# Kernel tuning notes

Hardware: AMD Instinct MI355X
Metric: run time of the kernel (lower is better)

The kernel has to match this reference:

```python
import jax, jax.numpy as jnp
import numpy as np

N_NEAR = 16
BN_EPS = 1e-5


def fps(xyz, n_center):
    # farthest point sampling, deterministic start at index 0. xyz: [B,N,C]
    B, N, _ = xyz.shape
    dist0 = jnp.full((B, N), jnp.inf, dtype=xyz.dtype)
    far0 = jnp.zeros((B,), dtype=jnp.int32)

    def step(carry, _):
        dist, far = carry
        centroid = jnp.take_along_axis(xyz, far[:, None, None], axis=1)  # [B,1,C]
        d = jnp.sum((xyz - centroid) ** 2, axis=-1)                       # [B,N]
        dist = jnp.minimum(dist, d)
        nxt = jnp.argmax(dist, axis=-1).astype(jnp.int32)
        return (dist, nxt), far

    _, idxs = jax.lax.scan(step, (dist0, far0), None, length=n_center)
    return jnp.transpose(idxs)  # [B, n_center]


def knn(xyz, k):
    # k nearest neighbors (self included), xyz: [B,N,C] -> idx [B,N,k]
    sq = jnp.sum(xyz * xyz, axis=-1)
    d = sq[:, :, None] - 2.0 * jnp.einsum('bnc,bmc->bnm', xyz, xyz) + sq[:, None, :]
    _, idx = jax.lax.top_k(-d, k)
    return idx


def gather_points(x, idx):
    # x: [B,N,...], idx: [B,*dims] int -> [B,*dims,...]
    return jax.vmap(lambda xb, ib: xb[ib])(x, idx)


def conv_bn_relu(x, W, b, g, be):
    # x: [B,C,K,S]; 1x1 Conv2d + BatchNorm2d (training/batch stats) + ReLU
    y = jnp.einsum('oc,bcks->boks', W, x) + b[None, :, None, None]
    mean = jnp.mean(y, axis=(0, 2, 3), keepdims=True)
    var = jnp.mean((y - mean) ** 2, axis=(0, 2, 3), keepdims=True)  # biased var, as torch BN
    y = (y - mean) * jax.lax.rsqrt(var + BN_EPS)
    y = y * g[None, :, None, None] + be[None, :, None, None]
    return jax.nn.relu(y)


def setup_inputs() -> dict:
    key = jax.random.key(0)
    ks = jax.random.split(key, 8)
    B, N, EMB = 16, 2048, 64
    mlp = [64, 128, 256]
    in_ch = 2 + EMB
    inp = {
        'xy': jax.random.normal(ks[0], (B, 2, N), dtype=jnp.float32),
        'fea': jax.random.normal(ks[1], (B, EMB, N), dtype=jnp.float32),
    }
    last = in_ch
    for i, out in enumerate(mlp):
        inp[f'W{i+1}'] = 0.1 * jax.random.normal(ks[2 + i], (out, last), dtype=jnp.float32)
        inp[f'b{i+1}'] = jnp.zeros((out,), dtype=jnp.float32)
        inp[f'g{i+1}'] = jnp.ones((out,), dtype=jnp.float32)
        inp[f'be{i+1}'] = jnp.zeros((out,), dtype=jnp.float32)
        last = out
    return inp


def reference(xy, fea, W1, b1, g1, be1, W2, b2, g2, be2, W3, b3, g3, be3):
    B, _, N = xy.shape
    n_center = N // 2 + 1
    xyz = jnp.transpose(xy, (0, 2, 1))   # [B,N,2]
    f = jnp.transpose(fea, (0, 2, 1))    # [B,N,emb]

    fps_idx = fps(xyz, n_center)                      # [B,S]
    new_xyz = gather_points(xyz, fps_idx)             # [B,S,2]
    knn_idx = knn(xyz, N_NEAR)                        # [B,N,k]
    knn_of_fps = gather_points(knn_idx, fps_idx)      # [B,S,k]
    grouped_xyz = gather_points(xyz, knn_of_fps)      # [B,S,k,2]
    grouped_norm = grouped_xyz - new_xyz[:, :, None, :]
    grouped_f = gather_points(f, knn_of_fps)          # [B,S,k,emb]
    new_fea = jnp.concatenate([grouped_norm, grouped_f], axis=-1)  # [B,S,k,C]

    x = jnp.transpose(new_fea, (0, 3, 2, 1))          # [B,C,k,S]
    for (W, b, g, be) in ((W1, b1, g1, be1), (W2, b2, g2, be2), (W3, b3, g3, be3)):
        x = conv_bn_relu(x, W, b, g, be)
    out = jnp.max(x, axis=2)                          # [B,C_out,S]
    return jnp.transpose(new_xyz, (0, 2, 1)), out
```

## Files before the change

### kernel.cpp

```cpp
#include <hip/hip_runtime.h>
#include <math.h>

#define B_   16
#define N_   2048
#define S_   1025
#define K_   16
#define EMB_ 64
#define NF_  (B_ * S_ * K_)
#define NCH_ (NF_ / 64)

typedef float v2f __attribute__((ext_vector_type(2)));
typedef short bf16x8 __attribute__((ext_vector_type(8)));
typedef float f32x4 __attribute__((ext_vector_type(4)));

__device__ __forceinline__ unsigned short f2bf(float f) {
  unsigned u = __float_as_uint(f);
  u += 0x7fffu + ((u >> 16) & 1u);
  return (unsigned short)(u >> 16);
}

__global__ __launch_bounds__(256) __attribute__((amdgpu_waves_per_eu(1, 1)))
void fps_pk_kernel(const float* __restrict__ xy, const float* __restrict__ fea,
                   const float* __restrict__ W1,
                   const float* __restrict__ W2, const float* __restrict__ W3,
                   int* __restrict__ fps_idx, float* __restrict__ new_xyz,
                   float* __restrict__ out0, float* __restrict__ P,
                   unsigned short* __restrict__ W2b, unsigned short* __restrict__ W3b) {
  __shared__ float smem[8192];
  if (blockIdx.x < 16) {
    const int b = blockIdx.x;
    float2* lxy = reinterpret_cast<float2*>(smem);
    const int lane = threadIdx.x;
    const float* xb = xy + (size_t)b * 2 * N_;
    v2f pxp[16], pyp[16];
    float dist[32];
    if (lane < 64) {
      const float2* xb2 = (const float2*)xb;
      const float2* yb2 = (const float2*)(xb + N_);
#pragma unroll
      for (int q = 0; q < 16; ++q) {
        float2 x01 = xb2[lane * 16 + q];
        float2 y01 = yb2[lane * 16 + q];
        int p = lane * 32 + 2 * q;
        lxy[p] = make_float2(x01.x, y01.x);
        lxy[p + 1] = make_float2(x01.y, y01.y);
        pxp[q][0] = x01.x; pxp[q][1] = x01.y;
        pyp[q][0] = y01.x; pyp[q][1] = y01.y;
        dist[2 * q] = __builtin_inff();
        dist[2 * q + 1] = __builtin_inff();
      }
#pragma unroll
      for (int q = 0; q < 16; ++q) {
        asm volatile("" : "+v"(pxp[q]), "+v"(pyp[q]));
      }
    }
    __syncthreads();
    if (lane < 64) {
      int cur = 0;
      for (int t = 0; t < S_; ++t) {
        float2 c = lxy[cur];
        if (lane == 0) {
          fps_idx[b * S_ + t] = cur;
          new_xyz[(b * S_ + t) * 2 + 0] = c.x;
          new_xyz[(b * S_ + t) * 2 + 1] = c.y;
          out0[b * 2 * S_ + t] = c.x;
          out0[b * 2 * S_ + S_ + t] = c.y;
        }
        const float ncx = -c.x, ncy = -c.y;
        v2f ncx2; ncx2[0] = ncx; ncx2[1] = ncx;
        v2f ncy2; ncy2[0] = ncy; ncy2[1] = ncy;
#pragma unroll
        for (int q = 0; q < 16; ++q) {
          v2f dx, dy, sx, sy, dd;
          asm("v_pk_add_f32 %0, %1, %2" : "=v"(dx) : "v"(pxp[q]), "v"(ncx2));
          asm("v_pk_add_f32 %0, %1, %2" : "=v"(dy) : "v"(pyp[q]), "v"(ncy2));
          asm("v_pk_mul_f32 %0, %1, %1" : "=v"(sx) : "v"(dx));
          asm("v_pk_mul_f32 %0, %1, %1" : "=v"(sy) : "v"(dy));
          asm("v_pk_add_f32 %0, %1, %2" : "=v"(dd) : "v"(sx), "v"(sy));
          dist[2 * q] = fminf(dist[2 * q], dd[0]);
          dist[2 * q + 1] = fminf(dist[2 * q + 1], dd[1]);
        }
        float m1[16], m2[8], m3[4], m4[2];
#pragma unroll
        for (int j = 0; j < 16; ++j) m1[j] = fmaxf(dist[2 * j], dist[2 * j + 1]);
#pragma unroll
        for (int j = 0; j < 8; ++j) m2[j] = fmaxf(m1[2 * j], m1[2 * j + 1]);
#pragma unroll
        for (int j = 0; j < 4; ++j) m3[j] = fmaxf(m2[2 * j], m2[2 * j + 1]);
        m4[0] = fmaxf(m3[0], m3[1]);
        m4[1] = fmaxf(m3[2], m3[3]);
        const float lmax = fmaxf(m4[0], m4[1]);
        int xr = __float_as_int(lmax);
#define DPP_MAX_STEP(CTRL)                                                        \
        {                                                                         \
          int tmp_ = __builtin_amdgcn_update_dpp(xr, xr, (CTRL), 0xF, 0xF, false);\
          xr = __float_as_int(fmaxf(__int_as_float(xr), __int_as_float(tmp_)));   \
        }
        DPP_MAX_STEP(0x111)
        DPP_MAX_STEP(0x112)
        DPP_MAX_STEP(0x114)
        DPP_MAX_STEP(0x118)
        DPP_MAX_STEP(0x142)
        DPP_MAX_STEP(0x143)
#undef DPP_MAX_STEP
        const float g = __int_as_float(__builtin_amdgcn_readlane(xr, 63));
        int n = (m4[0] == g) ? 0 : 1;
        float c3 = (n & 1) ? m3[2] : m3[0];
        n = 2 * n + ((c3 == g) ? 0 : 1);
        float lo2 = (n & 1) ? m2[2] : m2[0];
        float hi2 = (n & 1) ? m2[6] : m2[4];
        float c2 = (n & 2) ? hi2 : lo2;
        n = 2 * n + ((c2 == g) ? 0 : 1);
        float a0 = (n & 1) ? m1[2] : m1[0];
        float a1 = (n & 1) ? m1[6] : m1[4];
        float a2 = (n & 1) ? m1[10] : m1[8];
        float a3 = (n & 1) ? m1[14] : m1[12];
        float b0 = (n & 2) ? a1 : a0;
        float b1 = (n & 2) ? a3 : a2;
        float c1 = (n & 4) ? b1 : b0;
        n = 2 * n + ((c1 == g) ? 0 : 1);
        float e0 = (n & 1) ? dist[2] : dist[0];
        float e1 = (n & 1) ? dist[6] : dist[4];
        float e2 = (n & 1) ? dist[10] : dist[8];
        float e3 = (n & 1) ? dist[14] : dist[12];
        float e4 = (n & 1) ? dist[18] : dist[16];
        float e5 = (n & 1) ? dist[22] : dist[20];
        float e6 = (n & 1) ? dist[26] : dist[24];
        float e7 = (n & 1) ? dist[30] : dist[28];
        float f0 = (n & 2) ? e1 : e0;
        float f1 = (n & 2) ? e3 : e2;
        float f2 = (n & 2) ? e5 : e4;
        float f3 = (n & 2) ? e7 : e6;
        float g0 = (n & 4) ? f1 : f0;
        float g1 = (n & 4) ? f3 : f2;
        float c0 = (n & 8) ? g1 : g0;
        const int lf = 2 * n + ((c0 == g) ? 0 : 1);
        unsigned long long mask = __ballot(lmax == g);
        int first = __ffsll(mask) - 1;
        cur = __builtin_amdgcn_readlane(lane * 32 + lf, first);
      }
    }
  } else if (blockIdx.x < 528) {
    const int bid = blockIdx.x - 16;
    const int t = threadIdx.x;
    const int b = bid >> 5;
    const int pt0 = (bid & 31) << 6;
    float* W1L = smem;
    float* feaL = smem + 4096;
#pragma unroll
    for (int p = 0; p < 16; ++p) {
      int idx = t + 256 * p;
      int c = idx >> 6, e = idx & 63;
      W1L[e * 64 + c] = W1[c * 66 + 2 + e];
      int r = (t >> 6) + 4 * p, cc = t & 63;
      feaL[r * 64 + cc] = fea[((size_t)b * 64 + r) * N_ + pt0 + cc];
    }
    __syncthreads();
    const int tpt = t & 15, tcq = t >> 4;
    float acc[4][4];
#pragma unroll
    for (int i = 0; i < 4; ++i)
#pragma unroll
      for (int j = 0; j < 4; ++j) acc[i][j] = 0.f;
    for (int e = 0; e < 64; ++e) {
      float4 a4 = *reinterpret_cast<const float4*>(&W1L[e * 64 + tcq * 4]);
      float4 b4 = *reinterpret_cast<const float4*>(&feaL[e * 64 + tpt * 4]);
      const float av[4] = {a4.x, a4.y, a4.z, a4.w};
      const float bvv[4] = {b4.x, b4.y, b4.z, b4.w};
#pragma unroll
      for (int i = 0; i < 4; ++i)
#pragma unroll
        for (int j = 0; j < 4; ++j) acc[i][j] = fmaf(av[i], bvv[j], acc[i][j]);
    }
#pragma unroll
    for (int j = 0; j < 4; ++j) {
      int pt = tpt * 4 + j;
      float4 v = {acc[0][j], acc[1][j], acc[2][j], acc[3][j]};
      *reinterpret_cast<float4*>(&P[((size_t)(b * N_ + pt0 + pt)) * 64 + tcq * 4]) = v;
    }
  } else {
    const int t = threadIdx.x;
    for (int i = t; i < 128 * 64; i += 256) W2b[i] = f2bf(W2[i]);
    for (int i = t; i < 256 * 128; i += 256) W3b[i] = f2bf(W3[i]);
  }
}

__global__ __launch_bounds__(256) void knn_kernel(const float* __restrict__ xy,
                                                  const int* __restrict__ fps_idx,
                                                  int* __restrict__ knn_sel) {
  const int b = blockIdx.y;
  __shared__ float2 lxy[N_];
  __shared__ double lsq[N_];
  const float* xb = xy + (size_t)b * 2 * N_;
  for (int p = threadIdx.x; p < N_; p += 256) {
    float x = xb[p], y = xb[N_ + p];
    lxy[p] = make_float2(x, y);
    lsq[p] = (double)x * (double)x + (double)y * (double)y;
  }
  __syncthreads();
  const int t = threadIdx.x;
  const int s = blockIdx.x * 8 + (t >> 5);
  if (s >= S_) return;
  const int oct = t & 31;
  const int p0 = fps_idx[b * S_ + s];
  float2 q = lxy[p0];
  const double xn = (double)q.x, yn = (double)q.y;
  const double sqn = lsq[p0];
  double d16[16];
  int i16[16];
#pragma unroll
  for (int j = 0; j < 16; ++j) { d16[j] = __builtin_inf(); i16[j] = 0x7fffffff; }
  const int mlo = oct * 64;
  for (int m0 = mlo; m0 < mlo + 64; m0 += 4) {
    double dd[4];
#pragma unroll
    for (int u = 0; u < 4; ++u) {
      float2 p = lxy[m0 + u];
      double dot = (double)p.x * xn + (double)p.y * yn;
      dd[u] = (sqn - 2.0 * dot) + lsq[m0 + u];
    }
#pragma unroll
    for (int u = 0; u < 4; ++u) {
      if (dd[u] < d16[15]) {
        double d = dd[u];
        int mi = m0 + u;
#pragma unroll
        for (int j = 15; j >= 1; --j) {
          bool shift = d < d16[j - 1];
          bool ins = d < d16[j];
          d16[j] = shift ? d16[j - 1] : (ins ? d : d16[j]);
          i16[j] = shift ? i16[j - 1] : (ins ? mi : i16[j]);
        }
        if (d < d16[0]) { d16[0] = d; i16[0] = mi; }
      }
    }
  }
#pragma unroll
  for (int w = 1; w <= 16; w <<= 1) {
    double nd[16]; int ni[16];
#pragma unroll
    for (int i = 0; i < 16; ++i) {
      double rd = __shfl_xor(d16[15 - i], w, 64);
      int ri = __shfl_xor(i16[15 - i], w, 64);
      bool takeR = (rd < d16[i]) || (rd == d16[i] && ri < i16[i]);
      nd[i] = takeR ? rd : d16[i];
      ni[i] = takeR ? ri : i16[i];
    }
#pragma unroll
    for (int i = 0; i < 16; ++i) { d16[i] = nd[i]; i16[i] = ni[i]; }
    if (w < 16) {
#pragma unroll
      for (int dstg = 8; dstg >= 1; dstg >>= 1) {
#pragma unroll
        for (int i = 0; i < 16; ++i) {
          if ((i & dstg) == 0) {
            int a = i, c = i + dstg;
            bool sw = (d16[a] > d16[c]) || (d16[a] == d16[c] && i16[a] > i16[c]);
            double tlo = sw ? d16[c] : d16[a];
            double thi = sw ? d16[a] : d16[c];
            int ulo = sw ? i16[c] : i16[a];
            int uhi = sw ? i16[a] : i16[c];
            d16[a] = tlo; d16[c] = thi; i16[a] = ulo; i16[c] = uhi;
          }
        }
      }
    }
  }
  if (oct == 0) {
    int* dst = knn_sel + ((size_t)b * S_ + s) * K_;
#pragma unroll
    for (int j = 0; j < 16; ++j) dst[j] = i16[j];
  }
}

__global__ __launch_bounds__(256) void yk1_kernel(const float* __restrict__ xy,
                                                  const int* __restrict__ knn_sel,
                                                  const float* __restrict__ new_xyz,
                                                  const float* __restrict__ P,
                                                  const float* __restrict__ W1,
                                                  const float* __restrict__ b1,
                                                  float* __restrict__ Y1) {
  __shared__ float w0s[64], w1s[64], bbs[64];
  const int t = threadIdx.x;
  if (t < 64) { w0s[t] = W1[t * 66 + 0]; w1s[t] = W1[t * 66 + 1]; bbs[t] = b1[t]; }
  __syncthreads();
  const int n = blockIdx.x * 256 + t;
  const int bs = n >> 4;
  const int b = bs / S_;
  const int nbr = knn_sel[n];
  const float dx = xy[(size_t)b * 2 * N_ + nbr] - new_xyz[bs * 2 + 0];
  const float dy = xy[(size_t)b * 2 * N_ + N_ + nbr] - new_xyz[bs * 2 + 1];
  const float* prow = &P[((size_t)(b * N_ + nbr)) * 64];
  for (int c4 = 0; c4 < 64; c4 += 4) {
    float4 p4 = *reinterpret_cast<const float4*>(&prow[c4]);
    float v0 = p4.x + w0s[c4 + 0] * dx + w1s[c4 + 0] * dy + bbs[c4 + 0];
    float v1 = p4.y + w0s[c4 + 1] * dx + w1s[c4 + 1] * dy + bbs[c4 + 1];
    float v2 = p4.z + w0s[c4 + 2] * dx + w1s[c4 + 2] * dy + bbs[c4 + 2];
    float v3 = p4.w + w0s[c4 + 3] * dx + w1s[c4 + 3] * dy + bbs[c4 + 3];
    Y1[(size_t)(c4 + 0) * NF_ + n] = v0;
    Y1[(size_t)(c4 + 1) * NF_ + n] = v1;
    Y1[(size_t)(c4 + 2) * NF_ + n] = v2;
    Y1[(size_t)(c4 + 3) * NF_ + n] = v3;
  }
}

__global__ __launch_bounds__(256) void rowstats_kernel(const float* __restrict__ Y,
                                                       float* __restrict__ parts) {
  const int r = blockIdx.x & 63;
  const int qtr = blockIdx.x >> 6;
  const int QLEN = NF_ / 4;
  const float* seg = Y + (size_t)r * NF_ + (size_t)qtr * QLEN;
  double s = 0.0, s2 = 0.0;
  for (int i = threadIdx.x * 4; i < QLEN; i += 1024) {
    float4 v = *reinterpret_cast<const float4*>(&seg[i]);
    double dx = v.x, dy = v.y, dz = v.z, dw = v.w;
    s += (dx + dy) + (dz + dw);
    s2 = fma(dx, dx, s2); s2 = fma(dy, dy, s2);
    s2 = fma(dz, dz, s2); s2 = fma(dw, dw, s2);
  }
  __shared__ double sh[256], sh2[256];
  sh[threadIdx.x] = s; sh2[threadIdx.x] = s2;
  __syncthreads();
  for (int o = 128; o > 0; o >>= 1) {
    if (threadIdx.x < o) {
      sh[threadIdx.x] += sh[threadIdx.x + o];
      sh2[threadIdx.x] += sh2[threadIdx.x + o];
    }
    __syncthreads();
  }
  if (threadIdx.x == 0) {
    parts[(size_t)qtr * 128 + r] = (float)sh[0];
    parts[(size_t)qtr * 128 + 64 + r] = (float)sh2[0];
  }
}

__global__ void redabsch_kernel(const float* __restrict__ parts, int P, int M,
                                const float* __restrict__ g, const float* __restrict__ be,
                                float* __restrict__ A, float* __restrict__ D) {
  int m = threadIdx.x;
  if (m >= M) return;
  double a = 0.0, b = 0.0;
  for (int p = 0; p < P; ++p) {
    a += (double)parts[(size_t)p * 2 * M + m];
    b += (double)parts[(size_t)p * 2 * M + M + m];
  }
  double mu = a * (1.0 / NF_);
  double var = b * (1.0 / NF_) - mu * mu;
  double aa = (double)g[m] / sqrt(var + 1e-5);
  A[m] = (float)aa;
  D[m] = (float)((double)be[m] - aa * mu);
}

__device__ __forceinline__ float rowsum16(float v) {
#define RADD(CTRL) { int tm_ = __builtin_amdgcn_update_dpp(0, __float_as_int(v), (CTRL), 0xF, 0xF, true); \
                     v += __int_as_float(tm_); }
  RADD(0x111) RADD(0x112) RADD(0x114) RADD(0x118)
#undef RADD
  return v;
}

__global__ __launch_bounds__(256) void passA_mfma_kernel(
    const float* __restrict__ Y1, const unsigned short* __restrict__ W2b,
    const float* __restrict__ A1v, const float* __restrict__ Bc1v,
    float* __restrict__ parts) {
  __shared__ float ab1[128];
  __shared__ __align__(16) unsigned short x1b[64 * 64];
  const int t = threadIdx.x;
  const int w = t >> 6, L = t & 63;
  if (t < 128) ab1[t] = (t < 64) ? A1v[t] : Bc1v[t - 64];
  bf16x8 w2f[2][2];
#pragma unroll
  for (int rb = 0; rb < 2; ++rb)
#pragma unroll
    for (int ks = 0; ks < 2; ++ks) {
      int row = (2 * w + rb) * 16 + (L & 15);
      int koff = ks * 32 + (L >> 4) * 8;
      w2f[rb][ks] = *reinterpret_cast<const bf16x8*>(&W2b[row * 64 + koff]);
    }
  float vs[2][4], vq[2][4];
#pragma unroll
  for (int rb = 0; rb < 2; ++rb)
#pragma unroll
    for (int r = 0; r < 4; ++r) { vs[rb][r] = 0.f; vq[rb][r] = 0.f; }
  char* x1c = reinterpret_cast<char*>(x1b);
  for (int ch = blockIdx.x; ch < NCH_; ch += 512) {
    const size_t n0 = (size_t)ch * 64;
    __syncthreads();
#pragma unroll
    for (int e = 0; e < 8; ++e) {
      int k0 = 2 * (w + 4 * e);
      float y0 = Y1[(size_t)k0 * NF_ + n0 + L];
      float y1 = Y1[(size_t)(k0 + 1) * NF_ + n0 + L];
      float v0 = fmaxf(fmaf(y0, ab1[k0], ab1[64 + k0]), 0.f);
      float v1 = fmaxf(fmaf(y1, ab1[k0 + 1], ab1[64 + k0 + 1]), 0.f);
      unsigned pk = (unsigned)f2bf(v0) | ((unsigned)f2bf(v1) << 16);
      *reinterpret_cast<unsigned*>(&x1c[L * 128 + ((2 * k0) ^ ((L & 7) << 4))]) = pk;
    }
    __syncthreads();
#pragma unroll
    for (int rb = 0; rb < 2; ++rb) {
      f32x4 acc2[4];
#pragma unroll
      for (int cb = 0; cb < 4; ++cb) acc2[cb][0] = acc2[cb][1] = acc2[cb][2] = acc2[cb][3] = 0.f;
#pragma unroll
      for (int ks = 0; ks < 2; ++ks)
#pragma unroll
        for (int cb = 0; cb < 4; ++cb) {
          int n = cb * 16 + (L & 15);
          int koff = ks * 32 + (L >> 4) * 8;
          bf16x8 bfr = *reinterpret_cast<const bf16x8*>(&x1c[n * 128 + ((2 * koff) ^ ((n & 7) << 4))]);
          acc2[cb] = __builtin_amdgcn_mfma_f32_16x16x32_bf16(w2f[rb][ks], bfr, acc2[cb], 0, 0, 0);
        }
#pragma unroll
      for (int cb = 0; cb < 4; ++cb)
#pragma unroll
        for (int r = 0; r < 4; ++r) {
          float y = acc2[cb][r];
          vs[rb][r] += y;
          vq[rb][r] = fmaf(y, y, vq[rb][r]);
        }
    }
  }
#pragma unroll
  for (int rb = 0; rb < 2; ++rb)
#pragma unroll
    for (int r = 0; r < 4; ++r) {
      float s = rowsum16(vs[rb][r]);
      float q = rowsum16(vq[rb][r]);
      if ((L & 15) == 15) {
        int row = (2 * w + rb) * 16 + (L >> 4) * 4 + r;
        parts[(size_t)blockIdx.x * 256 + row] = s;
        parts[(size_t)blockIdx.x * 256 + 128 + row] = q;
      }
    }
}

__global__ __launch_bounds__(256) void passB_mfma_kernel(
    const float* __restrict__ Y1,
    const unsigned short* __restrict__ W2b, const unsigned short* __restrict__ W3b,
    const float* __restrict__ A1v, const float* __restrict__ Bc1v,
    const float* __restrict__ A2v, const float* __restrict__ D2v,
    float* __restrict__ parts) {
  __shared__ float ab1[128];
  __shared__ __align__(16) unsigned short x1b[64 * 64];
  __shared__ __align__(16) unsigned short x2b[64 * 128];
  const int t = threadIdx.x;
  const int w = t >> 6, L = t & 63;
  if (t < 128) ab1[t] = (t < 64) ? A1v[t] : Bc1v[t - 64];
  bf16x8 w3f[4][4];
#pragma unroll
  for (int rb = 0; rb < 4; ++rb)
#pragma unroll
    for (int ks = 0; ks < 4; ++ks) {
      int row = (4 * w + rb) * 16 + (L & 15);
      int koff = ks * 32 + (L >> 4) * 8;
      w3f[rb][ks] = *reinterpret_cast<const bf16x8*>(&W3b[row * 128 + koff]);
    }
  bf16x8 w2f[2][2];
#pragma unroll
  for (int rb = 0; rb < 2; ++rb)
#pragma unroll
    for (int ks = 0; ks < 2; ++ks) {
      int row = (2 * w + rb) * 16 + (L & 15);
      int koff = ks * 32 + (L >> 4) * 8;
      w2f[rb][ks] = *reinterpret_cast<const bf16x8*>(&W2b[row * 64 + koff]);
    }
  float vs[4][4], vq[4][4];
#pragma unroll
  for (int rb = 0; rb < 4; ++rb)
#pragma unroll
    for (int r = 0; r < 4; ++r) { vs[rb][r] = 0.f; vq[rb][r] = 0.f; }
  char* x1c = reinterpret_cast<char*>(x1b);
  char* x2c = reinterpret_cast<char*>(x2b);
  for (int ch = blockIdx.x; ch < NCH_; ch += 256) {
    const size_t n0 = (size_t)ch * 64;
    __syncthreads();
#pragma unroll
    for (int e = 0; e < 8; ++e) {
      int k0 = 2 * (w + 4 * e);
      float y0 = Y1[(size_t)k0 * NF_ + n0 + L];
      float y1 = Y1[(size_t)(k0 + 1) * NF_ + n0 + L];
      float v0 = fmaxf(fmaf(y0, ab1[k0], ab1[64 + k0]), 0.f);
      float v1 = fmaxf(fmaf(y1, ab1[k0 + 1], ab1[64 + k0 + 1]), 0.f);
      unsigned pk = (unsigned)f2bf(v0) | ((unsigned)f2bf(v1) << 16);
      *reinterpret_cast<unsigned*>(&x1c[L * 128 + ((2 * k0) ^ ((L & 7) << 4))]) = pk;
    }
    __syncthreads();
#pragma unroll
    for (int rb = 0; rb < 2; ++rb) {
      f32x4 acc2[4];
#pragma unroll
      for (int cb = 0; cb < 4; ++cb) acc2[cb][0] = acc2[cb][1] = acc2[cb][2] = acc2[cb][3] = 0.f;
#pragma unroll
      for (int ks = 0; ks < 2; ++ks)
#pragma unroll
        for (int cb = 0; cb < 4; ++cb) {
          int n = cb * 16 + (L & 15);
          int koff = ks * 32 + (L >> 4) * 8;
          bf16x8 bfr = *reinterpret_cast<const bf16x8*>(&x1c[n * 128 + ((2 * koff) ^ ((n & 7) << 4))]);
          acc2[cb] = __builtin_amdgcn_mfma_f32_16x16x32_bf16(w2f[rb][ks], bfr, acc2[cb], 0, 0, 0);
        }
#pragma unroll
      for (int cb = 0; cb < 4; ++cb) {
        int n = cb * 16 + (L & 15);
        int kbase = (2 * w + rb) * 16 + (L >> 4) * 4;
#pragma unroll
        for (int rp = 0; rp < 2; ++rp) {
          int r0 = 2 * rp;
          float a0 = A2v[kbase + r0], d0 = D2v[kbase + r0];
          float a1 = A2v[kbase + r0 + 1], d1 = D2v[kbase + r0 + 1];
          float v0 = fmaxf(fmaf(acc2[cb][r0], a0, d0), 0.f);
          float v1 = fmaxf(fmaf(acc2[cb][r0 + 1], a1, d1), 0.f);
          unsigned pk = (unsigned)f2bf(v0) | ((unsigned)f2bf(v1) << 16);
          int k0 = kbase + r0;
          *reinterpret_cast<unsigned*>(&x2c[n * 256 + ((2 * k0) ^ ((n & 7) << 4))]) = pk;
        }
      }
    }
    __syncthreads();
    bf16x8 b3[4][4];
#pragma unroll
    for (int cb = 0; cb < 4; ++cb)
#pragma unroll
      for (int ks = 0; ks < 4; ++ks) {
        int n = cb * 16 + (L & 15);
        int koff = ks * 32 + (L >> 4) * 8;
        b3[cb][ks] = *reinterpret_cast<const bf16x8*>(&x2c[n * 256 + ((2 * koff) ^ ((n & 7) << 4))]);
      }
#pragma unroll
    for (int rb = 0; rb < 4; ++rb) {
      f32x4 acc3[4];
#pragma unroll
      for (int cb = 0; cb < 4; ++cb) acc3[cb][0] = acc3[cb][1] = acc3[cb][2] = acc3[cb][3] = 0.f;
#pragma unroll
      for (int ks = 0; ks < 4; ++ks)
#pragma unroll
        for (int cb = 0; cb < 4; ++cb)
          acc3[cb] = __builtin_amdgcn_mfma_f32_16x16x32_bf16(w3f[rb][ks], b3[cb][ks], acc3[cb], 0, 0, 0);
#pragma unroll
      for (int cb = 0; cb < 4; ++cb)
#pragma unroll
        for (int r = 0; r < 4; ++r) {
          float y = acc3[cb][r];
          vs[rb][r] += y;
          vq[rb][r] = fmaf(y, y, vq[rb][r]);
        }
    }
  }
#pragma unroll
  for (int rb = 0; rb < 4; ++rb)
#pragma unroll
    for (int r = 0; r < 4; ++r) {
      float s = rowsum16(vs[rb][r]);
      float q = rowsum16(vq[rb][r]);
      if ((L & 15) == 15) {
        int row = (4 * w + rb) * 16 + (L >> 4) * 4 + r;
        parts[(size_t)blockIdx.x * 512 + row] = s;
        parts[(size_t)blockIdx.x * 512 + 256 + row] = q;
      }
    }
}

__global__ __launch_bounds__(256) void final_mfma_kernel(
    const float* __restrict__ Y1,
    const unsigned short* __restrict__ W2b,
    const unsigned short* __restrict__ W3b,
    const float* __restrict__ A1v, const float* __restrict__ Bc1v,
    const float* __restrict__ A2v, const float* __restrict__ D2v,
    const float* __restrict__ A3v, const float* __restrict__ D3v,
    float* __restrict__ out1) {
  __shared__ float ab1[128];
  __shared__ __align__(16) unsigned short x1b[64 * 64];
  __shared__ __align__(16) unsigned short x2b[64 * 128];
  const int t = threadIdx.x;
  const int w = t >> 6, L = t & 63;
  if (t < 128) ab1[t] = (t < 64) ? A1v[t] : Bc1v[t - 64];
  bf16x8 w3f[4][4];
#pragma unroll
  for (int rb = 0; rb < 4; ++rb)
#pragma unroll
    for (int ks = 0; ks < 4; ++ks) {
      int row = (4 * w + rb) * 16 + (L & 15);
      int koff = ks * 32 + (L >> 4) * 8;
      w3f[rb][ks] = *reinterpret_cast<const bf16x8*>(&W3b[row * 128 + koff]);
    }
  bf16x8 w2f[2][2];
#pragma unroll
  for (int rb = 0; rb < 2; ++rb)
#pragma unroll
    for (int ks = 0; ks < 2; ++ks) {
      int row = (2 * w + rb) * 16 + (L & 15);
      int koff = ks * 32 + (L >> 4) * 8;
      w2f[rb][ks] = *reinterpret_cast<const bf16x8*>(&W2b[row * 64 + koff]);
    }
  char* x1c = reinterpret_cast<char*>(x1b);
  char* x2c = reinterpret_cast<char*>(x2b);
  for (int ch = blockIdx.x; ch < NCH_; ch += 512) {
    const size_t n0 = (size_t)ch * 64;
    __syncthreads();
#pragma unroll
    for (int e = 0; e < 8; ++e) {
      int k0 = 2 * (w + 4 * e);
      float y0 = Y1[(size_t)k0 * NF_ + n0 + L];
      float y1 = Y1[(size_t)(k0 + 1) * NF_ + n0 + L];
      float v0 = fmaxf(fmaf(y0, ab1[k0], ab1[64 + k0]), 0.f);
      float v1 = fmaxf(fmaf(y1, ab1[k0 + 1], ab1[64 + k0 + 1]), 0.f);
      unsigned pk = (unsigned)f2bf(v0) | ((unsigned)f2bf(v1) << 16);
      *reinterpret_cast<unsigned*>(&x1c[L * 128 + ((2 * k0) ^ ((L & 7) << 4))]) = pk;
    }
    __syncthreads();
#pragma unroll
    for (int rb = 0; rb < 2; ++rb) {
      f32x4 acc2[4];
#pragma unroll
      for (int cb = 0; cb < 4; ++cb) acc2[cb][0] = acc2[cb][1] = acc2[cb][2] = acc2[cb][3] = 0.f;
#pragma unroll
      for (int ks = 0; ks < 2; ++ks)
#pragma unroll
        for (int cb = 0; cb < 4; ++cb) {
          int n = cb * 16 + (L & 15);
          int koff = ks * 32 + (L >> 4) * 8;
          bf16x8 bfr = *reinterpret_cast<const bf16x8*>(&x1c[n * 128 + ((2 * koff) ^ ((n & 7) << 4))]);
          acc2[cb] = __builtin_amdgcn_mfma_f32_16x16x32_bf16(w2f[rb][ks], bfr, acc2[cb], 0, 0, 0);
        }
#pragma unroll
      for (int cb = 0; cb < 4; ++cb) {
        int n = cb * 16 + (L & 15);
        int kbase = (2 * w + rb) * 16 + (L >> 4) * 4;
#pragma unroll
        for (int rp = 0; rp < 2; ++rp) {
          int r0 = 2 * rp;
          float a0 = A2v[kbase + r0], d0 = D2v[kbase + r0];
          float a1 = A2v[kbase + r0 + 1], d1 = D2v[kbase + r0 + 1];
          float v0 = fmaxf(fmaf(acc2[cb][r0], a0, d0), 0.f);
          float v1 = fmaxf(fmaf(acc2[cb][r0 + 1], a1, d1), 0.f);
          unsigned pk = (unsigned)f2bf(v0) | ((unsigned)f2bf(v1) << 16);
          int k0 = kbase + r0;
          *reinterpret_cast<unsigned*>(&x2c[n * 256 + ((2 * k0) ^ ((n & 7) << 4))]) = pk;
        }
      }
    }
    __syncthreads();
    bf16x8 b3[4][4];
#pragma unroll
    for (int cb = 0; cb < 4; ++cb)
#pragma unroll
      for (int ks = 0; ks < 4; ++ks) {
        int n = cb * 16 + (L & 15);
        int koff = ks * 32 + (L >> 4) * 8;
        b3[cb][ks] = *reinterpret_cast<const bf16x8*>(&x2c[n * 256 + ((2 * koff) ^ ((n & 7) << 4))]);
      }
#pragma unroll
    for (int rb = 0; rb < 4; ++rb) {
      f32x4 acc3[4];
#pragma unroll
      for (int cb = 0; cb < 4; ++cb) acc3[cb][0] = acc3[cb][1] = acc3[cb][2] = acc3[cb][3] = 0.f;
#pragma unroll
      for (int ks = 0; ks < 4; ++ks)
#pragma unroll
        for (int cb = 0; cb < 4; ++cb)
          acc3[cb] = __builtin_amdgcn_mfma_f32_16x16x32_bf16(w3f[rb][ks], b3[cb][ks], acc3[cb], 0, 0, 0);
      int rowbase = (4 * w + rb) * 16 + (L >> 4) * 4;
#pragma unroll
      for (int cb = 0; cb < 4; ++cb) {
#pragma unroll
        for (int r = 0; r < 4; ++r) {
          float v = fmaf(acc3[cb][r], A3v[rowbase + r], D3v[rowbase + r]);
          int xi = __float_as_int(v);
#define RMAX(CTRL) { int tm_ = __builtin_amdgcn_update_dpp(xi, xi, (CTRL), 0xF, 0xF, false); \
                     xi = __float_as_int(fmaxf(__int_as_float(xi), __int_as_float(tm_))); }
          RMAX(0x111) RMAX(0x112) RMAX(0x114) RMAX(0x118)
#undef RMAX
          if ((L & 15) == 15) {
            int row = rowbase + r;
            int bs = ch * 4 + cb;
            int b = bs / S_;
            int s = bs - b * S_;
            out1[((size_t)(b * 256 + row)) * S_ + s] = fmaxf(__int_as_float(xi), 0.f);
          }
        }
      }
    }
  }
}

__global__ void diag_kernel(float* out, float v) {
  if (threadIdx.x == 0 && blockIdx.x == 0) out[0] = v;
}

extern "C" void kernel_launch(void* const* d_in, const int* in_sizes, int n_in,
                              void* d_out, int out_size, void* d_ws, size_t ws_size,
                              hipStream_t stream) {
  const float* xy  = (const float*)d_in[0];
  const float* fea = (const float*)d_in[1];
  const float* W1  = (const float*)d_in[2];
  const float* b1  = (const float*)d_in[3];
  const float* g1  = (const float*)d_in[4];
  const float* be1 = (const float*)d_in[5];
  const float* W2  = (const float*)d_in[6];
  const float* g2  = (const float*)d_in[8];
  const float* be2 = (const float*)d_in[9];
  const float* W3  = (const float*)d_in[10];
  const float* g3  = (const float*)d_in[12];
  const float* be3 = (const float*)d_in[13];
  float* out = (float*)d_out;
  float* out1 = out + B_ * 2 * S_;

  char* w = (char*)d_ws;
  size_t off = 0;
  auto take = [&](size_t bytes) -> void* {
    void* p = w + off;
    off += (bytes + 255) & ~(size_t)255;
    return p;
  };
  int*    fps_idx = (int*)take((size_t)B_ * S_ * 4);
  float*  new_xyz = (float*)take((size_t)B_ * S_ * 2 * 4);
  int*    knn_sel = (int*)take((size_t)NF_ * 4);
  float*  P       = (float*)take((size_t)B_ * N_ * 64 * 4);
  float*  Y1      = (float*)take((size_t)64 * NF_ * 4);
  float*  parts1  = (float*)take((size_t)4 * 128 * 4);
  float*  A1      = (float*)take(64 * 4);
  float*  Bc1     = (float*)take(64 * 4);
  float*  partsA  = (float*)take((size_t)512 * 256 * 4);
  float*  A2      = (float*)take(128 * 4);
  float*  D2      = (float*)take(128 * 4);
  float*  partsB  = (float*)take((size_t)256 * 512 * 4);
  float*  A3      = (float*)take(256 * 4);
  float*  D3      = (float*)take(256 * 4);
  unsigned short* W2b = (unsigned short*)take((size_t)128 * 64 * 2);
  unsigned short* W3b = (unsigned short*)take((size_t)256 * 128 * 2);

  if (off > ws_size) {
    diag_kernel<<<1, 64, 0, stream>>>(out, (float)(ws_size >> 20));
    return;
  }

  fps_pk_kernel<<<16 + 512 + 1, 256, 0, stream>>>(xy, fea, W1, W2, W3,
                                                  fps_idx, new_xyz, out, P, W2b, W3b);
  knn_kernel<<<dim3((S_ + 7) / 8, B_), 256, 0, stream>>>(xy, fps_idx, knn_sel);
  yk1_kernel<<<NF_ / 256, 256, 0, stream>>>(xy, knn_sel, new_xyz, P, W1, b1, Y1);

  rowstats_kernel<<<256, 256, 0, stream>>>(Y1, parts1);
  redabsch_kernel<<<1, 64, 0, stream>>>(parts1, 4, 64, g1, be1, A1, Bc1);

  passA_mfma_kernel<<<512, 256, 0, stream>>>(Y1, W2b, A1, Bc1, partsA);
  redabsch_kernel<<<1, 128, 0, stream>>>(partsA, 512, 128, g2, be2, A2, D2);

  passB_mfma_kernel<<<256, 256, 0, stream>>>(Y1, W2b, W3b, A1, Bc1, A2, D2, partsB);
  redabsch_kernel<<<1, 256, 0, stream>>>(partsB, 256, 256, g3, be3, A3, D3);

  final_mfma_kernel<<<512, 256, 0, stream>>>(Y1, W2b, W3b, A1, Bc1, A2, D2, A3, D3, out1);
}
```

Baseline: 1.343 ms.

## Compute KNN for all points concurrently with FPS instead of after it

The separate KNN launch, which depended on FPS indices, is removed. KNN is now computed for every point (2048 per batch rather than 1025 FPS centers) inside extra blocks of the FPS kernel, so it can overlap with the serial FPS loop that occupies only 16 blocks. yk1 then looks up neighbors through fps_idx into the full KNN table. This roughly doubles KNN work and adds an indirection, in exchange for hiding KNN behind the long-running FPS blocks and dropping one launch.

Measured after the change: 1.801 ms. 34.1% more time.

```diff
diff --git a/kernel.cpp b/kernel.cpp
--- a/kernel.cpp
+++ b/kernel.cpp
@@ -25,8 +25,9 @@
                    const float* __restrict__ W2, const float* __restrict__ W3,
                    int* __restrict__ fps_idx, float* __restrict__ new_xyz,
                    float* __restrict__ out0, float* __restrict__ P,
-                   unsigned short* __restrict__ W2b, unsigned short* __restrict__ W3b) {
-  __shared__ float smem[8192];
+                   unsigned short* __restrict__ W2b, unsigned short* __restrict__ W3b,
+                   int* __restrict__ knn_all) {
+  __shared__ __align__(16) float smem[8192];
   if (blockIdx.x < 16) {
     const int b = blockIdx.x;
     float2* lxy = reinterpret_cast<float2*>(smem);
@@ -178,103 +179,100 @@
       float4 v = {acc[0][j], acc[1][j], acc[2][j], acc[3][j]};
       *reinterpret_cast<float4*>(&P[((size_t)(b * N_ + pt0 + pt)) * 64 + tcq * 4]) = v;
     }
-  } else {
+  } else if (blockIdx.x == 528) {
     const int t = threadIdx.x;
     for (int i = t; i < 128 * 64; i += 256) W2b[i] = f2bf(W2[i]);
     for (int i = t; i < 256 * 128; i += 256) W3b[i] = f2bf(W3[i]);
-  }
-}
-
-__global__ __launch_bounds__(256) void knn_kernel(const float* __restrict__ xy,
+  } else {
+    const int kblk = blockIdx.x - 529;
+    const int b = kblk >> 8;
+    const int q0 = (kblk & 255) << 3;
+    float2* lxy = reinterpret_cast<float2*>(smem);
+    double* lsq = reinterpret_cast<double*>(smem + 4096);
+    const float* xb = xy + (size_t)b * 2 * N_;
+    for (int p = threadIdx.x; p < N_; p += 256) {
+      float x = xb[p], y = xb[N_ + p];
+      lxy[p] = make_float2(x, y);
+      lsq[p] = (double)x * (double)x + (double)y * (double)y;
+    }
+    __syncthreads();
+    const int t = threadIdx.x;
+    const int q = q0 + (t >> 5);
+    const int oct = t & 31;
+    float2 qq = lxy[q];
+    const double xn = (double)qq.x, yn = (double)qq.y;
+    const double sqn = lsq[q];
+    double d16[16];
+    int i16[16];
+#pragma unroll
+    for (int j = 0; j < 16; ++j) { d16[j] = __builtin_inf(); i16[j] = 0x7fffffff; }
+    const int mlo = oct * 64;
+    for (int m0 = mlo; m0 < mlo + 64; m0 += 4) {
+      double dd[4];
+#pragma unroll
+      for (int u = 0; u < 4; ++u) {
+        float2 p = lxy[m0 + u];
+        double dot = (double)p.x * xn + (double)p.y * yn;
+        dd[u] = (sqn - 2.0 * dot) + lsq[m0 + u];
+      }
+#pragma unroll
+      for (int u = 0; u < 4; ++u) {
+        if (dd[u] < d16[15]) {
+          double d = dd[u];
+          int mi = m0 + u;
+#pragma unroll
+          for (int j = 15; j >= 1; --j) {
+            bool shift = d < d16[j - 1];
+            bool ins = d < d16[j];
+            d16[j] = shift ? d16[j - 1] : (ins ? d : d16[j]);
+            i16[j] = shift ? i16[j - 1] : (ins ? mi : i16[j]);
+          }
+          if (d < d16[0]) { d16[0] = d; i16[0] = mi; }
+        }
+      }
+    }
+#pragma unroll
+    for (int w = 1; w <= 16; w <<= 1) {
+      double nd[16]; int ni[16];
+#pragma unroll
+      for (int i = 0; i < 16; ++i) {
+        double rd = __shfl_xor(d16[15 - i], w, 64);
+        int ri = __shfl_xor(i16[15 - i], w, 64);
+        bool takeR = (rd < d16[i]) || (rd == d16[i] && ri < i16[i]);
+        nd[i] = takeR ? rd : d16[i];
+        ni[i] = takeR ? ri : i16[i];
+      }
+#pragma unroll
+      for (int i = 0; i < 16; ++i) { d16[i] = nd[i]; i16[i] = ni[i]; }
+      if (w < 16) {
+#pragma unroll
+        for (int dstg = 8; dstg >= 1; dstg >>= 1) {
+#pragma unroll
+          for (int i = 0; i < 16; ++i) {
+            if ((i & dstg) == 0) {
+              int a = i, c = i + dstg;
+              bool sw = (d16[a] > d16[c]) || (d16[a] == d16[c] && i16[a] > i16[c]);
+              double tlo = sw ? d16[c] : d16[a];
+              double thi = sw ? d16[a] : d16[c];
+              int ulo = sw ? i16[c] : i16[a];
+              int uhi = sw ? i16[a] : i16[c];
+              d16[a] = tlo; d16[c] = thi; i16[a] = ulo; i16[c] = uhi;
+            }
+          }
+        }
+      }
+    }
+    if (oct == 0) {
+      int* dst = knn_all + ((size_t)b * N_ + q) * K_;
+#pragma unroll
+      for (int j = 0; j < 16; ++j) dst[j] = i16[j];
+    }
+  }
+}
+
+__global__ __launch_bounds__(256) void yk1_kernel(const float* __restrict__ xy,
                                                   const int* __restrict__ fps_idx,
-                                                  int* __restrict__ knn_sel) {
-  const int b = blockIdx.y;
-  __shared__ float2 lxy[N_];
-  __shared__ double lsq[N_];
-  const float* xb = xy + (size_t)b * 2 * N_;
-  for (int p = threadIdx.x; p < N_; p += 256) {
-    float x = xb[p], y = xb[N_ + p];
-    lxy[p] = make_float2(x, y);
-    lsq[p] = (double)x * (double)x + (double)y * (double)y;
-  }
-  __syncthreads();
-  const int t = threadIdx.x;
-  const int s = blockIdx.x * 8 + (t >> 5);
-  if (s >= S_) return;
-  const int oct = t & 31;
-  const int p0 = fps_idx[b * S_ + s];
-  float2 q = lxy[p0];
-  const double xn = (double)q.x, yn = (double)q.y;
-  const double sqn = lsq[p0];
-  double d16[16];
-  int i16[16];
-#pragma unroll
-  for (int j = 0; j < 16; ++j) { d16[j] = __builtin_inf(); i16[j] = 0x7fffffff; }
-  const int mlo = oct * 64;
-  for (int m0 = mlo; m0 < mlo + 64; m0 += 4) {
-    double dd[4];
-#pragma unroll
-    for (int u = 0; u < 4; ++u) {
-      float2 p = lxy[m0 + u];
-      double dot = (double)p.x * xn + (double)p.y * yn;
-      dd[u] = (sqn - 2.0 * dot) + lsq[m0 + u];
-    }
-#pragma unroll
-    for (int u = 0; u < 4; ++u) {
-      if (dd[u] < d16[15]) {
-        double d = dd[u];
-        int mi = m0 + u;
-#pragma unroll
-        for (int j = 15; j >= 1; --j) {
-          bool shift = d < d16[j - 1];
-          bool ins = d < d16[j];
-          d16[j] = shift ? d16[j - 1] : (ins ? d : d16[j]);
-          i16[j] = shift ? i16[j - 1] : (ins ? mi : i16[j]);
-        }
-        if (d < d16[0]) { d16[0] = d; i16[0] = mi; }
-      }
-    }
-  }
-#pragma unroll
-  for (int w = 1; w <= 16; w <<= 1) {
-    double nd[16]; int ni[16];
-#pragma unroll
-    for (int i = 0; i < 16; ++i) {
-      double rd = __shfl_xor(d16[15 - i], w, 64);
-      int ri = __shfl_xor(i16[15 - i], w, 64);
-      bool takeR = (rd < d16[i]) || (rd == d16[i] && ri < i16[i]);
-      nd[i] = takeR ? rd : d16[i];
-      ni[i] = takeR ? ri : i16[i];
-    }
-#pragma unroll
-    for (int i = 0; i < 16; ++i) { d16[i] = nd[i]; i16[i] = ni[i]; }
-    if (w < 16) {
-#pragma unroll
-      for (int dstg = 8; dstg >= 1; dstg >>= 1) {
-#pragma unroll
-        for (int i = 0; i < 16; ++i) {
-          if ((i & dstg) == 0) {
-            int a = i, c = i + dstg;
-            bool sw = (d16[a] > d16[c]) || (d16[a] == d16[c] && i16[a] > i16[c]);
-            double tlo = sw ? d16[c] : d16[a];
-            double thi = sw ? d16[a] : d16[c];
-            int ulo = sw ? i16[c] : i16[a];
-            int uhi = sw ? i16[a] : i16[c];
-            d16[a] = tlo; d16[c] = thi; i16[a] = ulo; i16[c] = uhi;
-          }
-        }
-      }
-    }
-  }
-  if (oct == 0) {
-    int* dst = knn_sel + ((size_t)b * S_ + s) * K_;
-#pragma unroll
-    for (int j = 0; j < 16; ++j) dst[j] = i16[j];
-  }
-}
-
-__global__ __launch_bounds__(256) void yk1_kernel(const float* __restrict__ xy,
-                                                  const int* __restrict__ knn_sel,
+                                                  const int* __restrict__ knn_all,
                                                   const float* __restrict__ new_xyz,
                                                   const float* __restrict__ P,
                                                   const float* __restrict__ W1,
@@ -287,7 +285,9 @@
   const int n = blockIdx.x * 256 + t;
   const int bs = n >> 4;
   const int b = bs / S_;
-  const int nbr = knn_sel[n];
+  const int s = bs - b * S_;
+  const int p0 = fps_idx[b * S_ + s];
+  const int nbr = knn_all[((size_t)b * N_ + p0) * K_ + (n & 15)];
   const float dx = xy[(size_t)b * 2 * N_ + nbr] - new_xyz[bs * 2 + 0];
   const float dy = xy[(size_t)b * 2 * N_ + N_ + nbr] - new_xyz[bs * 2 + 1];
   const float* prow = &P[((size_t)(b * N_ + nbr)) * 64];
@@ -715,7 +715,7 @@
   };
   int*    fps_idx = (int*)take((size_t)B_ * S_ * 4);
   float*  new_xyz = (float*)take((size_t)B_ * S_ * 2 * 4);
-  int*    knn_sel = (int*)take((size_t)NF_ * 4);
+  int*    knn_all = (int*)take((size_t)B_ * N_ * K_ * 4);
   float*  P       = (float*)take((size_t)B_ * N_ * 64 * 4);
   float*  Y1      = (float*)take((size_t)64 * NF_ * 4);
   float*  parts1  = (float*)take((size_t)4 * 128 * 4);
@@ -735,10 +735,9 @@
     return;
   }
 
-  fps_pk_kernel<<<16 + 512 + 1, 256, 0, stream>>>(xy, fea, W1, W2, W3,
-                                                  fps_idx, new_xyz, out, P, W2b, W3b);
-  knn_kernel<<<dim3((S_ + 7) / 8, B_), 256, 0, stream>>>(xy, fps_idx, knn_sel);
-  yk1_kernel<<<NF_ / 256, 256, 0, stream>>>(xy, knn_sel, new_xyz, P, W1, b1, Y1);
+  fps_pk_kernel<<<16 + 512 + 1 + 4096, 256, 0, stream>>>(
+      xy, fea, W1, W2, W3, fps_idx, new_xyz, out, P, W2b, W3b, knn_all);
+  yk1_kernel<<<NF_ / 256, 256, 0, stream>>>(xy, fps_idx, knn_all, new_xyz, P, W1, b1, Y1);
 
   rowstats_kernel<<<256, 256, 0, stream>>>(Y1, parts1);
   redabsch_kernel<<<1, 64, 0, stream>>>(parts1, 4, 64, g1, be1, A1, Bc1);
```

## Record per-group max/min of layer-3 pre-BN output to skip final recompute

Applied to the files above, without the earlier changes.

During the layer-3 statistics pass, each 16-neighbor group's max and min of the pre-BN conv output are reduced with DPP and stored as a packed bf16 pair. Because BN followed by ReLU is monotone per channel, the output can then come from a small elementwise kernel that picks max or min by the sign of the BN scale. This removes a full recompute of layers 1-3 through MFMA in the final kernel. In exchange it adds a scattered write of the extremes in passB, workspace pressure with a fallback to the old path, and bf16 rounding of the stored extremes.

Result: no change. 1.345 ms (+0.1%).

```diff
diff --git a/kernel.cpp b/kernel.cpp
--- a/kernel.cpp
+++ b/kernel.cpp
@@ -8,6 +8,7 @@
 #define EMB_ 64
 #define NF_  (B_ * S_ * K_)
 #define NCH_ (NF_ / 64)
+#define NBS_ (NCH_ * 4)
 
 typedef float v2f __attribute__((ext_vector_type(2)));
 typedef short bf16x8 __attribute__((ext_vector_type(8)));
@@ -440,7 +441,7 @@
     const unsigned short* __restrict__ W2b, const unsigned short* __restrict__ W3b,
     const float* __restrict__ A1v, const float* __restrict__ Bc1v,
     const float* __restrict__ A2v, const float* __restrict__ D2v,
-    float* __restrict__ parts) {
+    float* __restrict__ parts, unsigned* __restrict__ M3) {
   __shared__ float ab1[128];
   __shared__ __align__(16) unsigned short x1b[64 * 64];
   __shared__ __align__(16) unsigned short x2b[64 * 128];
@@ -545,6 +546,31 @@
           vs[rb][r] += y;
           vq[rb][r] = fmaf(y, y, vq[rb][r]);
         }
+      if (M3) {
+        int rowbase = (4 * w + rb) * 16 + (L >> 4) * 4;
+#pragma unroll
+        for (int cb = 0; cb < 4; ++cb) {
+#pragma unroll
+          for (int r = 0; r < 4; ++r) {
+            float v = acc3[cb][r];
+            int xi = __float_as_int(v), xm = __float_as_int(v);
+#define RMAX(CTRL) { int tm_ = __builtin_amdgcn_update_dpp(xi, xi, (CTRL), 0xF, 0xF, false); \
+                     xi = __float_as_int(fmaxf(__int_as_float(xi), __int_as_float(tm_))); }
+#define RMIN(CTRL) { int tm_ = __builtin_amdgcn_update_dpp(xm, xm, (CTRL), 0xF, 0xF, false); \
+                     xm = __float_as_int(fminf(__int_as_float(xm), __int_as_float(tm_))); }
+            RMAX(0x111) RMAX(0x112) RMAX(0x114) RMAX(0x118)
+            RMIN(0x111) RMIN(0x112) RMIN(0x114) RMIN(0x118)
+#undef RMAX
+#undef RMIN
+            if ((L & 15) == 15) {
+              int row = rowbase + r;
+              int bs = ch * 4 + cb;
+              M3[(size_t)row * NBS_ + bs] =
+                  (unsigned)f2bf(__int_as_float(xi)) | ((unsigned)f2bf(__int_as_float(xm)) << 16);
+            }
+          }
+        }
+      }
     }
   }
 #pragma unroll
@@ -559,6 +585,20 @@
         parts[(size_t)blockIdx.x * 512 + 256 + row] = q;
       }
     }
+}
+
+__global__ __launch_bounds__(256) void final_small_kernel(
+    const unsigned* __restrict__ M3, const float* __restrict__ A3,
+    const float* __restrict__ D3, float* __restrict__ out1) {
+  int gid = blockIdx.x * 256 + threadIdx.x;
+  int row = gid / NBS_, bs = gid - row * NBS_;
+  unsigned pk = M3[gid];
+  float vmax = __uint_as_float((pk & 0xffffu) << 16);
+  float vmin = __uint_as_float(pk & 0xffff0000u);
+  float a = A3[row];
+  float v = (a >= 0.f) ? vmax : vmin;
+  int b = bs / S_, s = bs - b * S_;
+  out1[((size_t)(b * 256 + row)) * S_ + s] = fmaxf(fmaf(v, a, D3[row]), 0.f);
 }
 
 __global__ __launch_bounds__(256) void final_mfma_kernel(
@@ -729,11 +769,16 @@
   float*  D3      = (float*)take(256 * 4);
   unsigned short* W2b = (unsigned short*)take((size_t)128 * 64 * 2);
   unsigned short* W3b = (unsigned short*)take((size_t)256 * 128 * 2);
-
-  if (off > ws_size) {
+  size_t base_off = off;
+
+  if (base_off > ws_size) {
     diag_kernel<<<1, 64, 0, stream>>>(out, (float)(ws_size >> 20));
     return;
   }
+
+  unsigned* M3 = (unsigned*)take((size_t)256 * NBS_ * 4);
+  bool haveM3 = (off <= ws_size);
+  if (!haveM3) M3 = nullptr;
 
   fps_pk_kernel<<<16 + 512 + 1, 256, 0, stream>>>(xy, fea, W1, W2, W3,
                                                   fps_idx, new_xyz, out, P, W2b, W3b);
@@ -746,8 +791,12 @@
   passA_mfma_kernel<<<512, 256, 0, stream>>>(Y1, W2b, A1, Bc1, partsA);
   redabsch_kernel<<<1, 128, 0, stream>>>(partsA, 512, 128, g2, be2, A2, D2);
 
-  passB_mfma_kernel<<<256, 256, 0, stream>>>(Y1, W2b, W3b, A1, Bc1, A2, D2, partsB);
+  passB_mfma_kernel<<<256, 256, 0, stream>>>(Y1, W2b, W3b, A1, Bc1, A2, D2, partsB, M3);
   redabsch_kernel<<<1, 256, 0, stream>>>(partsB, 256, 256, g3, be3, A3, D3);
 
-  final_mfma_kernel<<<512, 256, 0, stream>>>(Y1, W2b, W3b, A1, Bc1, A2, D2, A3, D3, out1);
-}
+  if (haveM3) {
+    final_small_kernel<<<(256 * NBS_) / 256, 256, 0, stream>>>(M3, A3, D3, out1);
+  } else {
+    final_mfma_kernel<<<512, 256, 0, stream>>>(Y1, W2b, W3b, A1, Bc1, A2, D2, A3, D3, out1);
+  }
+}
```
